# Kernel tuning notes

Measured on AMD Instinct MI355X. Metric: run time of the kernel, lower is better.

Reference implementation:

```python
import jax, jax.numpy as jnp
import numpy as np

HEADS = 8
DIM_HEAD = 64
INNER = HEADS * DIM_HEAD  # 512
EPS = 1e-6


def layer_norm(x, gamma, beta):
    mu = jnp.mean(x, axis=-1, keepdims=True)
    var = jnp.var(x, axis=-1, keepdims=True)
    return (x - mu) * jax.lax.rsqrt(var + EPS) * gamma + beta


def setup_inputs() -> dict:
    key = jax.random.key(0)
    ks = jax.random.split(key, 8)
    b, n = 2, 2048
    s = lambda d: 1.0 / np.sqrt(d)
    return {
        "x": jax.random.normal(ks[0], (b, n, INNER), dtype=jnp.float32),
        # weights stored input-major: y = x @ W
        "w_qkv": jax.random.normal(ks[1], (INNER, 3 * INNER), dtype=jnp.float32) * s(INNER),
        "w_out": jax.random.normal(ks[2], (INNER, INNER), dtype=jnp.float32) * s(INNER),
        "b_out": jax.random.normal(ks[3], (INNER,), dtype=jnp.float32) * 0.01,
        "w_ff1": jax.random.normal(ks[4], (INNER, 4 * INNER), dtype=jnp.float32) * s(INNER),
        "w_ff2": jax.random.normal(ks[5], (4 * INNER, INNER), dtype=jnp.float32) * s(4 * INNER),
        "g1": jnp.ones((INNER,), dtype=jnp.float32),
        "be1": jnp.zeros((INNER,), dtype=jnp.float32),
        "g2": jnp.ones((INNER,), dtype=jnp.float32),
        "be2": jnp.zeros((INNER,), dtype=jnp.float32),
    }


def reference(x, w_qkv, w_out, b_out, w_ff1, w_ff2, g1, be1, g2, be2):
    b, n, _ = x.shape
    scale = DIM_HEAD ** (-0.5)
    qkv = x @ w_qkv  # [b, n, 3*inner]
    qkv = qkv.reshape(b, n, 3, HEADS, DIM_HEAD)
    q = qkv[:, :, 0].transpose(0, 2, 1, 3)  # [b, h, n, d]
    k = qkv[:, :, 1].transpose(0, 2, 1, 3)
    v = qkv[:, :, 2].transpose(0, 2, 1, 3)
    dots = jnp.einsum('bhqd,bhkd->bhqk', q, k) * scale
    attn = jax.nn.softmax(dots, axis=-1)
    out = jnp.einsum('bhqk,bhkd->bhqd', attn, v)
    out = out.transpose(0, 2, 1, 3).reshape(b, n, INNER)
    out = out @ w_out + b_out
    attn_res = layer_norm(x + out, g1, be1)
    # NOTE: no activation between the two FFN linears (faithful to source)
    ff = (attn_res @ w_ff1) @ w_ff2
    return layer_norm(attn_res + ff, g2, be2)
```

## Files before the change

### kernel.cpp

```cpp
#include <hip/hip_runtime.h>
#include <hip/hip_bf16.h>
#include <cstdint>
#include <cstddef>
#include <math.h>

#define HEADS 8
#define DHEAD 64
#define INNER 512
#define BATCH 2
#define SEQ   2048
#define MROWS (BATCH*SEQ)
#define LN_EPS 1e-6f
#define KSPLIT 2
#define KCHUNK (SEQ/KSPLIT)

typedef unsigned short u16;
typedef __attribute__((ext_vector_type(8))) short short8;
typedef __attribute__((ext_vector_type(4))) float f32x4;

#define MFMA16(a,b,c) __builtin_amdgcn_mfma_f32_16x16x32_bf16((a),(b),(c),0,0,0)

__device__ __forceinline__ float bf2f(u16 u) {
    union { float f; uint32_t i; } x; x.i = ((uint32_t)u) << 16; return x.f;
}
__device__ __forceinline__ u16 f2bf(float f) {
    __hip_bfloat16 h = __float2bfloat16(f);
    return *reinterpret_cast<u16*>(&h);
}
__device__ __forceinline__ void gl_lds16(const void* g, void* l) {
    __builtin_amdgcn_global_load_lds(
        (const __attribute__((address_space(1))) void*)g,
        (__attribute__((address_space(3))) void*)l, 16, 0, 0);
}

__global__ void f32_to_bf16_kernel(const float* __restrict__ in,
                                   u16* __restrict__ out, int n4) {
    int i = (blockIdx.x * 256 + threadIdx.x);
    if (i < n4) {
        float4 v = reinterpret_cast<const float4*>(in)[i];
        ushort4 o;
        o.x = f2bf(v.x); o.y = f2bf(v.y); o.z = f2bf(v.z); o.w = f2bf(v.w);
        reinterpret_cast<ushort4*>(out)[i] = o;
    }
}

__global__ void transpose_to_bf16_kernel(const float* __restrict__ B,
                                         u16* __restrict__ Bt, int K, int N) {
    __shared__ float T[32][33];
    const int tid = threadIdx.x;
    const int n0 = blockIdx.x * 32, k0 = blockIdx.y * 32;
    const int r = tid >> 3, c = (tid & 7) * 4;
    float4 v = *reinterpret_cast<const float4*>(&B[(size_t)(k0 + r) * N + n0 + c]);
    T[c + 0][r] = v.x; T[c + 1][r] = v.y; T[c + 2][r] = v.z; T[c + 3][r] = v.w;
    __syncthreads();
    ushort4 o;
    o.x = f2bf(T[r][c + 0]); o.y = f2bf(T[r][c + 1]);
    o.z = f2bf(T[r][c + 2]); o.w = f2bf(T[r][c + 3]);
    *reinterpret_cast<ushort4*>(&Bt[(size_t)(n0 + r) * K + k0 + c]) = o;
}

template<int BN, int EPI>
__global__ __launch_bounds__(256) void gemm_bt(const u16* __restrict__ A,
                                               const u16* __restrict__ Bt,
                                               const float* __restrict__ bias,
                                               float* __restrict__ C,
                                               u16* __restrict__ Cb,
                                               u16* __restrict__ Vt,
                                               int M, int N, int K) {
    constexpr int WN = BN / 2;
    constexpr int NT = WN / 16;
    __shared__ u16 As[128 * 32];
    __shared__ u16 Bs[BN * 32];
    const int tid = threadIdx.x;
    const int wave = tid >> 6, lane = tid & 63;
    const int l15 = lane & 15, quad = lane >> 4;
    const int wm = (wave >> 1) * 64, wn = (wave & 1) * WN;
    const int row0 = blockIdx.y * 128, col0 = blockIdx.x * BN;

    int kbase = 0, kend = K;
    if (EPI == 3) {
        int chunk = K / gridDim.z;
        kbase = blockIdx.z * chunk; kend = kbase + chunk;
    }

    f32x4 acc[4][NT];
    #pragma unroll
    for (int mi = 0; mi < 4; ++mi)
        #pragma unroll
        for (int ni = 0; ni < NT; ++ni)
            #pragma unroll
            for (int e = 0; e < 4; ++e) acc[mi][ni][e] = 0.f;

    for (int k0 = kbase; k0 < kend; k0 += 32) {
        #pragma unroll
        for (int idx0 = 0; idx0 < 512 + BN * 4; idx0 += 256) {
            int idx = idx0 + tid;
            if (idx < 512) {
                int r = idx >> 2, ic = (idx & 3) * 8;
                gl_lds16(A + (size_t)(row0 + r) * K + k0 + ic, &As[idx * 8]);
            } else {
                int ib = idx - 512;
                int r = ib >> 2, ic = (ib & 3) * 8;
                gl_lds16(Bt + (size_t)(col0 + r) * K + k0 + ic, &Bs[ib * 8]);
            }
        }
        __syncthreads();

        short8 af[4], bf[NT];
        #pragma unroll
        for (int mi = 0; mi < 4; ++mi)
            af[mi] = *reinterpret_cast<const short8*>(&As[(wm + mi * 16 + l15) * 32 + quad * 8]);
        #pragma unroll
        for (int ni = 0; ni < NT; ++ni)
            bf[ni] = *reinterpret_cast<const short8*>(&Bs[(wn + ni * 16 + l15) * 32 + quad * 8]);
        #pragma unroll
        for (int mi = 0; mi < 4; ++mi)
            #pragma unroll
            for (int ni = 0; ni < NT; ++ni)
                acc[mi][ni] = MFMA16(af[mi], bf[ni], acc[mi][ni]);
        __syncthreads();
    }

    #pragma unroll
    for (int mi = 0; mi < 4; ++mi)
        #pragma unroll
        for (int ni = 0; ni < NT; ++ni) {
            const int cc = col0 + wn + ni * 16 + l15;
            const int rr0 = row0 + wm + mi * 16 + quad * 4;
            if (EPI == 0) {
                #pragma unroll
                for (int r = 0; r < 4; ++r)
                    Cb[(size_t)(rr0 + r) * N + cc] = f2bf(acc[mi][ni][r]);
            } else if (EPI == 1) {
                #pragma unroll
                for (int r = 0; r < 4; ++r)
                    C[(size_t)(rr0 + r) * N + cc] = acc[mi][ni][r] + bias[cc];
            } else if (EPI == 3) {
                float* Cz = C + (size_t)blockIdx.z * M * N;
                #pragma unroll
                for (int r = 0; r < 4; ++r)
                    Cz[(size_t)(rr0 + r) * N + cc] = acc[mi][ni][r];
            } else {
                if (cc < 1024) {
                    size_t base = (cc < 512) ? (size_t)cc
                                             : ((size_t)MROWS * 512 + cc - 512);
                    #pragma unroll
                    for (int r = 0; r < 4; ++r)
                        Cb[base + (size_t)(rr0 + r) * 512] = f2bf(acc[mi][ni][r]);
                } else {
                    int hh = (cc - 1024) >> 6, dd = (cc - 1024) & 63;
                    int bb = rr0 >> 11, srow = rr0 & 2047;
                    ushort4 o;
                    o.x = f2bf(acc[mi][ni][0]); o.y = f2bf(acc[mi][ni][1]);
                    o.z = f2bf(acc[mi][ni][2]); o.w = f2bf(acc[mi][ni][3]);
                    *reinterpret_cast<ushort4*>(
                        &Vt[(((size_t)(bb * 8 + hh) * 64 + dd) << 11) + srow]) = o;
                }
            }
        }
}

__global__ __launch_bounds__(256) void attn_kernel(const u16* __restrict__ qk_b,
                                                   const u16* __restrict__ vT_b,
                                                   float* __restrict__ Opart,
                                                   float* __restrict__ lpart) {
    __shared__ u16 QP[64][72];
    __shared__ u16 Ks[64][72];
    __shared__ u16 VT[64][72];

    const int tid = threadIdx.x;
    const int wave = tid >> 6, lane = tid & 63;
    const int l15 = lane & 15, quad = lane >> 4;
    const int qt = blockIdx.x, bh = blockIdx.y, ks = blockIdx.z;
    const int b = bh >> 3, h = bh & 7;
    const int w16 = wave * 16;
    const int r0 = tid >> 3, r1 = r0 + 32;
    const int ch = (tid & 7) * 8;

    {
        const u16* qb = qk_b + (size_t)(b * SEQ + qt * 64) * 512 + h * 64;
        *reinterpret_cast<uint4*>(&QP[r0][ch]) =
            *reinterpret_cast<const uint4*>(&qb[(size_t)r0 * 512 + ch]);
        *reinterpret_cast<uint4*>(&QP[r1][ch]) =
            *reinterpret_cast<const uint4*>(&qb[(size_t)r1 * 512 + ch]);
    }
    __syncthreads();

    short8 qf[2];
    qf[0] = *reinterpret_cast<const short8*>(&QP[w16 + l15][quad * 8]);
    qf[1] = *reinterpret_cast<const short8*>(&QP[w16 + l15][32 + quad * 8]);

    f32x4 oacc[4];
    float lsum[4];
    #pragma unroll
    for (int di = 0; di < 4; ++di)
        #pragma unroll
        for (int e = 0; e < 4; ++e) oacc[di][e] = 0.f;
    #pragma unroll
    for (int r = 0; r < 4; ++r) lsum[r] = 0.f;

    const u16* kb = qk_b + (size_t)MROWS * 512
                  + (size_t)(b * SEQ + ks * KCHUNK) * 512 + h * 64;
    const u16* vb = vT_b + (size_t)bh * 64 * 2048 + ks * KCHUNK;

    uint4 kr0 = *reinterpret_cast<const uint4*>(&kb[(size_t)r0 * 512 + ch]);
    uint4 kr1 = *reinterpret_cast<const uint4*>(&kb[(size_t)r1 * 512 + ch]);
    uint4 vr0 = *reinterpret_cast<const uint4*>(&vb[(size_t)r0 * 2048 + ch]);
    uint4 vr1 = *reinterpret_cast<const uint4*>(&vb[(size_t)r1 * 2048 + ch]);

    const float CEXP = 0.18033688011110918f;

    for (int kt = 0; kt < KCHUNK / 64; ++kt) {
        *reinterpret_cast<uint4*>(&Ks[r0][ch]) = kr0;
        *reinterpret_cast<uint4*>(&Ks[r1][ch]) = kr1;
        *reinterpret_cast<uint4*>(&VT[r0][ch]) = vr0;
        *reinterpret_cast<uint4*>(&VT[r1][ch]) = vr1;
        __syncthreads();

        if (kt + 1 < KCHUNK / 64) {
            const u16* kb2 = kb + (size_t)(kt + 1) * 64 * 512;
            const u16* vb2 = vb + (kt + 1) * 64;
            kr0 = *reinterpret_cast<const uint4*>(&kb2[(size_t)r0 * 512 + ch]);
            kr1 = *reinterpret_cast<const uint4*>(&kb2[(size_t)r1 * 512 + ch]);
            vr0 = *reinterpret_cast<const uint4*>(&vb2[(size_t)r0 * 2048 + ch]);
            vr1 = *reinterpret_cast<const uint4*>(&vb2[(size_t)r1 * 2048 + ch]);
        }

        f32x4 sacc[4];
        #pragma unroll
        for (int ni = 0; ni < 4; ++ni)
            #pragma unroll
            for (int e = 0; e < 4; ++e) sacc[ni][e] = 0.f;
        #pragma unroll
        for (int ksk = 0; ksk < 2; ++ksk) {
            short8 kf[4];
            #pragma unroll
            for (int ni = 0; ni < 4; ++ni)
                kf[ni] = *reinterpret_cast<const short8*>(
                    &Ks[ni * 16 + l15][ksk * 32 + quad * 8]);
            #pragma unroll
            for (int ni = 0; ni < 4; ++ni)
                sacc[ni] = MFMA16(qf[ksk], kf[ni], sacc[ni]);
        }

        #pragma unroll
        for (int ni = 0; ni < 4; ++ni)
            #pragma unroll
            for (int r = 0; r < 4; ++r) {
                float p = exp2f(sacc[ni][r] * CEXP);
                lsum[r] += p;
                QP[w16 + quad * 4 + r][ni * 16 + l15] = f2bf(p);
            }

        #pragma unroll
        for (int ksk = 0; ksk < 2; ++ksk) {
            short8 pf = *reinterpret_cast<const short8*>(
                &QP[w16 + l15][ksk * 32 + quad * 8]);
            #pragma unroll
            for (int di = 0; di < 4; ++di) {
                short8 vf = *reinterpret_cast<const short8*>(
                    &VT[di * 16 + l15][ksk * 32 + quad * 8]);
                oacc[di] = MFMA16(pf, vf, oacc[di]);
            }
        }
        __syncthreads();
    }

    #pragma unroll
    for (int r = 0; r < 4; ++r) {
        float v = lsum[r];
        v += __shfl_xor(v, 1); v += __shfl_xor(v, 2);
        v += __shfl_xor(v, 4); v += __shfl_xor(v, 8);
        lsum[r] = v;
    }

    const size_t pbase = ((size_t)(ks * 16 + bh) * SEQ + qt * 64);
    #pragma unroll
    for (int di = 0; di < 4; ++di)
        #pragma unroll
        for (int r = 0; r < 4; ++r)
            Opart[(pbase + w16 + quad * 4 + r) * 64 + di * 16 + l15] = oacc[di][r];
    if (l15 == 0)
        #pragma unroll
        for (int r = 0; r < 4; ++r)
            lpart[pbase + w16 + quad * 4 + r] = lsum[r];
}

__global__ void attn_combine_kernel(const float* __restrict__ Opart,
                                    const float* __restrict__ lpart,
                                    u16* __restrict__ attn_b) {
    int i = blockIdx.x * 256 + threadIdx.x;
    int e = i * 4;
    int row = e >> 9;
    int c = e & 511;
    int h = c >> 6, d = c & 63;
    int b = row >> 11, srow = row & 2047;
    int bh = b * 8 + h;

    size_t i0 = ((size_t)bh * SEQ + srow) * 64 + d;
    size_t i1 = ((size_t)(16 + bh) * SEQ + srow) * 64 + d;
    float4 o0 = *reinterpret_cast<const float4*>(&Opart[i0]);
    float4 o1 = *reinterpret_cast<const float4*>(&Opart[i1]);
    float l = lpart[(size_t)bh * SEQ + srow] + lpart[(size_t)(16 + bh) * SEQ + srow];
    float li = 1.f / l;
    ushort4 o;
    o.x = f2bf((o0.x + o1.x) * li);
    o.y = f2bf((o0.y + o1.y) * li);
    o.z = f2bf((o0.z + o1.z) * li);
    o.w = f2bf((o0.w + o1.w) * li);
    *reinterpret_cast<ushort4*>(&attn_b[(size_t)row * INNER + c]) = o;
}

template<bool A16, bool TWO>
__global__ void ln_kernel(const void* __restrict__ a_,
                          const float* __restrict__ s0,
                          const float* __restrict__ s1,
                          const float* __restrict__ g,
                          const float* __restrict__ be,
                          float* __restrict__ out32,
                          u16* __restrict__ out16) {
    __shared__ float red[256];
    const int row = blockIdx.x, tid = threadIdx.x;
    const size_t off = (size_t)row * INNER;
    const int c0 = tid, c1 = tid + 256;

    float a0, a1;
    if (A16) {
        const u16* a = (const u16*)a_;
        a0 = bf2f(a[off + c0]); a1 = bf2f(a[off + c1]);
    } else {
        const float* a = (const float*)a_;
        a0 = a[off + c0]; a1 = a[off + c1];
    }
    float v0 = a0 + s0[off + c0];
    float v1 = a1 + s0[off + c1];
    if (TWO) { v0 += s1[off + c0]; v1 += s1[off + c1]; }

    red[tid] = v0 + v1;
    __syncthreads();
    for (int s = 128; s > 0; s >>= 1) {
        if (tid < s) red[tid] += red[tid + s];
        __syncthreads();
    }
    float mu = red[0] * (1.f / INNER);
    __syncthreads();

    float d0 = v0 - mu, d1 = v1 - mu;
    red[tid] = d0 * d0 + d1 * d1;
    __syncthreads();
    for (int s = 128; s > 0; s >>= 1) {
        if (tid < s) red[tid] += red[tid + s];
        __syncthreads();
    }
    float rstd = rsqrtf(red[0] * (1.f / INNER) + LN_EPS);

    float y0 = d0 * rstd * g[c0] + be[c0];
    float y1 = d1 * rstd * g[c1] + be[c1];
    if (out32) { out32[off + c0] = y0; out32[off + c1] = y1; }
    if (out16) { out16[off + c0] = f2bf(y0); out16[off + c1] = f2bf(y1); }
}

extern "C" void kernel_launch(void* const* d_in, const int* in_sizes, int n_in,
                              void* d_out, int out_size, void* d_ws, size_t ws_size,
                              hipStream_t stream) {
    const float* x     = (const float*)d_in[0];
    const float* w_qkv = (const float*)d_in[1];
    const float* w_out = (const float*)d_in[2];
    const float* b_out = (const float*)d_in[3];
    const float* w_ff1 = (const float*)d_in[4];
    const float* w_ff2 = (const float*)d_in[5];
    const float* g1    = (const float*)d_in[6];
    const float* be1   = (const float*)d_in[7];
    const float* g2    = (const float*)d_in[8];
    const float* be2   = (const float*)d_in[9];
    float* out = (float*)d_out;

    char* W = (char*)d_ws;
    u16*   w_outT     = (u16*)  (W + 0);
    u16*   w_ff1T     = (u16*)  (W + 524288);
    u16*   w_ff2T     = (u16*)  (W + 2621440);
    u16*   qk_b       = (u16*)  (W + 4718592);
    u16*   attn_b     = (u16*)  (W + 4718592);
    u16*   attn_res_b = (u16*)  (W + 4718592);
    float* proj       = (float*)(W + 8912896);
    u16*   ff1_b      = (u16*)  (W + 8912896);
    u16*   vT_b       = (u16*)  (W + 13107200);
    u16*   x_b        = (u16*)  (W + 17301504);
    u16*   w_qkvT     = (u16*)  (W + 21495808);
    float* Opart      = (float*)(W + 17301504);
    float* lpart      = (float*)(W + 34078720);
    float* ff2p       = (float*)(W + 25690112);

    f32_to_bf16_kernel<<<(MROWS * INNER / 4 + 255) / 256, 256, 0, stream>>>(
        x, x_b, MROWS * INNER / 4);
    transpose_to_bf16_kernel<<<dim3(1536 / 32, 512 / 32),  256, 0, stream>>>(w_qkv, w_qkvT, 512, 1536);
    transpose_to_bf16_kernel<<<dim3(512 / 32,  512 / 32),  256, 0, stream>>>(w_out, w_outT, 512, 512);
    transpose_to_bf16_kernel<<<dim3(2048 / 32, 512 / 32),  256, 0, stream>>>(w_ff1, w_ff1T, 512, 2048);
    transpose_to_bf16_kernel<<<dim3(512 / 32,  2048 / 32), 256, 0, stream>>>(w_ff2, w_ff2T, 2048, 512);

    gemm_bt<128, 2><<<dim3(1536 / 128, MROWS / 128), 256, 0, stream>>>(
        x_b, w_qkvT, nullptr, nullptr, qk_b, vT_b, MROWS, 1536, INNER);

    attn_kernel<<<dim3(SEQ / 64, BATCH * HEADS, KSPLIT), 256, 0, stream>>>(
        qk_b, vT_b, Opart, lpart);

    attn_combine_kernel<<<(MROWS * INNER / 4) / 256, 256, 0, stream>>>(
        Opart, lpart, attn_b);

    gemm_bt<64, 1><<<dim3(INNER / 64, MROWS / 128), 256, 0, stream>>>(
        attn_b, w_outT, b_out, proj, nullptr, nullptr, MROWS, INNER, INNER);

    ln_kernel<false, false><<<MROWS, 256, 0, stream>>>(
        x, proj, nullptr, g1, be1, nullptr, attn_res_b);

    gemm_bt<128, 0><<<dim3(2048 / 128, MROWS / 128), 256, 0, stream>>>(
        attn_res_b, w_ff1T, nullptr, nullptr, ff1_b, nullptr, MROWS, 2048, INNER);

    gemm_bt<64, 3><<<dim3(INNER / 64, MROWS / 128, 2), 256, 0, stream>>>(
        ff1_b, w_ff2T, nullptr, ff2p, nullptr, nullptr, MROWS, INNER, 2048);

    ln_kernel<true, true><<<MROWS, 256, 0, stream>>>(
        attn_res_b, ff2p, ff2p + (size_t)MROWS * INNER, g2, be2, out, nullptr);
}
```

Measured before the change: 236.0 us.

## Fuse prep kernels, split attention keys four ways, keep P in registers

After: 223.6 us. 5.3% less time.

```diff
diff --git a/kernel.cpp b/kernel.cpp
--- a/kernel.cpp
+++ b/kernel.cpp
@@ -11,14 +11,19 @@
 #define SEQ   2048
 #define MROWS (BATCH*SEQ)
 #define LN_EPS 1e-6f
-#define KSPLIT 2
+#define KSPLIT 4
 #define KCHUNK (SEQ/KSPLIT)
 
 typedef unsigned short u16;
 typedef __attribute__((ext_vector_type(8))) short short8;
+typedef __attribute__((ext_vector_type(4))) short short4v;
 typedef __attribute__((ext_vector_type(4))) float f32x4;
 
 #define MFMA16(a,b,c) __builtin_amdgcn_mfma_f32_16x16x32_bf16((a),(b),(c),0,0,0)
+#if __has_builtin(__builtin_amdgcn_mfma_f32_16x16x16bf16_1k)
+#define HAVE_MFMA16K16 1
+#define MFMA16K16(a,b,c) __builtin_amdgcn_mfma_f32_16x16x16bf16_1k((a),(b),(c),0,0,0)
+#endif
 
 __device__ __forceinline__ float bf2f(u16 u) {
     union { float f; uint32_t i; } x; x.i = ((uint32_t)u) << 16; return x.f;
@@ -33,22 +38,28 @@
         (__attribute__((address_space(3))) void*)l, 16, 0, 0);
 }
 
-__global__ void f32_to_bf16_kernel(const float* __restrict__ in,
-                                   u16* __restrict__ out, int n4) {
-    int i = (blockIdx.x * 256 + threadIdx.x);
-    if (i < n4) {
-        float4 v = reinterpret_cast<const float4*>(in)[i];
+__global__ void prep_kernel(const float* __restrict__ x, u16* __restrict__ x_b,
+                            const float* __restrict__ w_qkv, u16* __restrict__ w_qkvT,
+                            const float* __restrict__ w_out, u16* __restrict__ w_outT,
+                            const float* __restrict__ w_ff1, u16* __restrict__ w_ff1T,
+                            const float* __restrict__ w_ff2, u16* __restrict__ w_ff2T) {
+    __shared__ float T[32][33];
+    const int blk = blockIdx.x, tid = threadIdx.x;
+    if (blk < 2048) {
+        int i = blk * 256 + tid;
+        float4 v = reinterpret_cast<const float4*>(x)[i];
         ushort4 o;
         o.x = f2bf(v.x); o.y = f2bf(v.y); o.z = f2bf(v.z); o.w = f2bf(v.w);
-        reinterpret_cast<ushort4*>(out)[i] = o;
-    }
-}
-
-__global__ void transpose_to_bf16_kernel(const float* __restrict__ B,
-                                         u16* __restrict__ Bt, int K, int N) {
-    __shared__ float T[32][33];
-    const int tid = threadIdx.x;
-    const int n0 = blockIdx.x * 32, k0 = blockIdx.y * 32;
+        reinterpret_cast<ushort4*>(x_b)[i] = o;
+        return;
+    }
+    const float* B; u16* Bt; int K, N, t;
+    if (blk < 2816)      { B = w_qkv; Bt = w_qkvT; K = 512;  N = 1536; t = blk - 2048; }
+    else if (blk < 3072) { B = w_out; Bt = w_outT; K = 512;  N = 512;  t = blk - 2816; }
+    else if (blk < 4096) { B = w_ff1; Bt = w_ff1T; K = 512;  N = 2048; t = blk - 3072; }
+    else                 { B = w_ff2; Bt = w_ff2T; K = 2048; N = 512;  t = blk - 4096; }
+    const int nb = N / 32;
+    const int n0 = (t % nb) * 32, k0 = (t / nb) * 32;
     const int r = tid >> 3, c = (tid & 7) * 4;
     float4 v = *reinterpret_cast<const float4*>(&B[(size_t)(k0 + r) * N + n0 + c]);
     T[c + 0][r] = v.x; T[c + 1][r] = v.y; T[c + 2][r] = v.z; T[c + 3][r] = v.w;
@@ -162,11 +173,12 @@
 
 __global__ __launch_bounds__(256) void attn_kernel(const u16* __restrict__ qk_b,
                                                    const u16* __restrict__ vT_b,
-                                                   float* __restrict__ Opart,
+                                                   u16* __restrict__ OpartB,
                                                    float* __restrict__ lpart) {
-    __shared__ u16 QP[64][72];
-    __shared__ u16 Ks[64][72];
-    __shared__ u16 VT[64][72];
+    __shared__ u16 SM[3 * 64 * 72];
+    u16 (*Qs)[72] = (u16(*)[72])SM;
+    u16 (*Ks)[72] = (u16(*)[72])(SM + 64 * 72);
+    u16 (*VT)[72] = (u16(*)[72])(SM + 2 * 64 * 72);
 
     const int tid = threadIdx.x;
     const int wave = tid >> 6, lane = tid & 63;
@@ -179,25 +191,16 @@
 
     {
         const u16* qb = qk_b + (size_t)(b * SEQ + qt * 64) * 512 + h * 64;
-        *reinterpret_cast<uint4*>(&QP[r0][ch]) =
+        *reinterpret_cast<uint4*>(&Qs[r0][ch]) =
             *reinterpret_cast<const uint4*>(&qb[(size_t)r0 * 512 + ch]);
-        *reinterpret_cast<uint4*>(&QP[r1][ch]) =
+        *reinterpret_cast<uint4*>(&Qs[r1][ch]) =
             *reinterpret_cast<const uint4*>(&qb[(size_t)r1 * 512 + ch]);
     }
     __syncthreads();
 
     short8 qf[2];
-    qf[0] = *reinterpret_cast<const short8*>(&QP[w16 + l15][quad * 8]);
-    qf[1] = *reinterpret_cast<const short8*>(&QP[w16 + l15][32 + quad * 8]);
-
-    f32x4 oacc[4];
-    float lsum[4];
-    #pragma unroll
-    for (int di = 0; di < 4; ++di)
-        #pragma unroll
-        for (int e = 0; e < 4; ++e) oacc[di][e] = 0.f;
-    #pragma unroll
-    for (int r = 0; r < 4; ++r) lsum[r] = 0.f;
+    qf[0] = *reinterpret_cast<const short8*>(&Qs[w16 + l15][quad * 8]);
+    qf[1] = *reinterpret_cast<const short8*>(&Qs[w16 + l15][32 + quad * 8]);
 
     const u16* kb = qk_b + (size_t)MROWS * 512
                   + (size_t)(b * SEQ + ks * KCHUNK) * 512 + h * 64;
@@ -209,6 +212,14 @@
     uint4 vr1 = *reinterpret_cast<const uint4*>(&vb[(size_t)r1 * 2048 + ch]);
 
     const float CEXP = 0.18033688011110918f;
+
+#ifdef HAVE_MFMA16K16
+    f32x4 oacc[4];
+    float lsum = 0.f;
+    #pragma unroll
+    for (int di = 0; di < 4; ++di)
+        #pragma unroll
+        for (int e = 0; e < 4; ++e) oacc[di][e] = 0.f;
 
     for (int kt = 0; kt < KCHUNK / 64; ++kt) {
         *reinterpret_cast<uint4*>(&Ks[r0][ch]) = kr0;
@@ -240,22 +251,103 @@
                     &Ks[ni * 16 + l15][ksk * 32 + quad * 8]);
             #pragma unroll
             for (int ni = 0; ni < 4; ++ni)
+                sacc[ni] = MFMA16(kf[ni], qf[ksk], sacc[ni]);
+        }
+
+        #pragma unroll
+        for (int ni = 0; ni < 4; ++ni) {
+            short4v pp;
+            #pragma unroll
+            for (int r = 0; r < 4; ++r) {
+                float p = exp2f(sacc[ni][r] * CEXP);
+                lsum += p;
+                pp[r] = (short)f2bf(p);
+            }
+            #pragma unroll
+            for (int di = 0; di < 4; ++di) {
+                short4v vf = *reinterpret_cast<const short4v*>(
+                    &VT[di * 16 + l15][ni * 16 + quad * 4]);
+                oacc[di] = MFMA16K16(vf, pp, oacc[di]);
+            }
+        }
+        __syncthreads();
+    }
+
+    lsum += __shfl_xor(lsum, 16);
+    lsum += __shfl_xor(lsum, 32);
+
+    const size_t pbase = ((size_t)(ks * 16 + bh) * SEQ + qt * 64);
+    if (lane < 16) lpart[pbase + w16 + lane] = lsum;
+
+    float* OTf = (float*)SM;
+    #pragma unroll
+    for (int di = 0; di < 4; ++di)
+        #pragma unroll
+        for (int r = 0; r < 4; ++r)
+            OTf[(di * 16 + quad * 4 + r) * 68 + w16 + l15] = oacc[di][r];
+    __syncthreads();
+
+    const int ql = tid >> 2, dseg = (tid & 3) * 16;
+    u16 ov[16];
+    #pragma unroll
+    for (int i = 0; i < 16; ++i) ov[i] = f2bf(OTf[(dseg + i) * 68 + ql]);
+    u16* op = &OpartB[(pbase + ql) * 64 + dseg];
+    *reinterpret_cast<uint4*>(op)     = *reinterpret_cast<const uint4*>(ov);
+    *reinterpret_cast<uint4*>(op + 8) = *reinterpret_cast<const uint4*>(ov + 8);
+#else
+    f32x4 oacc[4];
+    float lsum[4];
+    #pragma unroll
+    for (int di = 0; di < 4; ++di)
+        #pragma unroll
+        for (int e = 0; e < 4; ++e) oacc[di][e] = 0.f;
+    #pragma unroll
+    for (int r = 0; r < 4; ++r) lsum[r] = 0.f;
+
+    for (int kt = 0; kt < KCHUNK / 64; ++kt) {
+        *reinterpret_cast<uint4*>(&Ks[r0][ch]) = kr0;
+        *reinterpret_cast<uint4*>(&Ks[r1][ch]) = kr1;
+        *reinterpret_cast<uint4*>(&VT[r0][ch]) = vr0;
+        *reinterpret_cast<uint4*>(&VT[r1][ch]) = vr1;
+        __syncthreads();
+
+        if (kt + 1 < KCHUNK / 64) {
+            const u16* kb2 = kb + (size_t)(kt + 1) * 64 * 512;
+            const u16* vb2 = vb + (kt + 1) * 64;
+            kr0 = *reinterpret_cast<const uint4*>(&kb2[(size_t)r0 * 512 + ch]);
+            kr1 = *reinterpret_cast<const uint4*>(&kb2[(size_t)r1 * 512 + ch]);
+            vr0 = *reinterpret_cast<const uint4*>(&vb2[(size_t)r0 * 2048 + ch]);
+            vr1 = *reinterpret_cast<const uint4*>(&vb2[(size_t)r1 * 2048 + ch]);
+        }
+
+        f32x4 sacc[4];
+        #pragma unroll
+        for (int ni = 0; ni < 4; ++ni)
+            #pragma unroll
+            for (int e = 0; e < 4; ++e) sacc[ni][e] = 0.f;
+        #pragma unroll
+        for (int ksk = 0; ksk < 2; ++ksk) {
+            short8 kf[4];
+            #pragma unroll
+            for (int ni = 0; ni < 4; ++ni)
+                kf[ni] = *reinterpret_cast<const short8*>(
+                    &Ks[ni * 16 + l15][ksk * 32 + quad * 8]);
+            #pragma unroll
+            for (int ni = 0; ni < 4; ++ni)
                 sacc[ni] = MFMA16(qf[ksk], kf[ni], sacc[ni]);
         }
-
         #pragma unroll
         for (int ni = 0; ni < 4; ++ni)
             #pragma unroll
             for (int r = 0; r < 4; ++r) {
                 float p = exp2f(sacc[ni][r] * CEXP);
                 lsum[r] += p;
-                QP[w16 + quad * 4 + r][ni * 16 + l15] = f2bf(p);
+                Qs[w16 + quad * 4 + r][ni * 16 + l15] = f2bf(p);
             }
-
         #pragma unroll
         for (int ksk = 0; ksk < 2; ++ksk) {
             short8 pf = *reinterpret_cast<const short8*>(
-                &QP[w16 + l15][ksk * 32 + quad * 8]);
+                &Qs[w16 + l15][ksk * 32 + quad * 8]);
             #pragma unroll
             for (int di = 0; di < 4; ++di) {
                 short8 vf = *reinterpret_cast<const short8*>(
@@ -273,20 +365,20 @@
         v += __shfl_xor(v, 4); v += __shfl_xor(v, 8);
         lsum[r] = v;
     }
-
     const size_t pbase = ((size_t)(ks * 16 + bh) * SEQ + qt * 64);
     #pragma unroll
     for (int di = 0; di < 4; ++di)
         #pragma unroll
         for (int r = 0; r < 4; ++r)
-            Opart[(pbase + w16 + quad * 4 + r) * 64 + di * 16 + l15] = oacc[di][r];
+            OpartB[(pbase + w16 + quad * 4 + r) * 64 + di * 16 + l15] = f2bf(oacc[di][r]);
     if (l15 == 0)
         #pragma unroll
         for (int r = 0; r < 4; ++r)
             lpart[pbase + w16 + quad * 4 + r] = lsum[r];
-}
-
-__global__ void attn_combine_kernel(const float* __restrict__ Opart,
+#endif
+}
+
+__global__ void attn_combine_kernel(const u16* __restrict__ OpartB,
                                     const float* __restrict__ lpart,
                                     u16* __restrict__ attn_b) {
     int i = blockIdx.x * 256 + threadIdx.x;
@@ -297,17 +389,18 @@
     int b = row >> 11, srow = row & 2047;
     int bh = b * 8 + h;
 
-    size_t i0 = ((size_t)bh * SEQ + srow) * 64 + d;
-    size_t i1 = ((size_t)(16 + bh) * SEQ + srow) * 64 + d;
-    float4 o0 = *reinterpret_cast<const float4*>(&Opart[i0]);
-    float4 o1 = *reinterpret_cast<const float4*>(&Opart[i1]);
-    float l = lpart[(size_t)bh * SEQ + srow] + lpart[(size_t)(16 + bh) * SEQ + srow];
+    float ax = 0.f, ay = 0.f, az = 0.f, aw = 0.f, l = 0.f;
+    #pragma unroll
+    for (int ks = 0; ks < KSPLIT; ++ks) {
+        size_t pk = (size_t)(ks * 16 + bh) * SEQ + srow;
+        ushort4 o = *reinterpret_cast<const ushort4*>(&OpartB[pk * 64 + d]);
+        ax += bf2f(o.x); ay += bf2f(o.y); az += bf2f(o.z); aw += bf2f(o.w);
+        l += lpart[pk];
+    }
     float li = 1.f / l;
     ushort4 o;
-    o.x = f2bf((o0.x + o1.x) * li);
-    o.y = f2bf((o0.y + o1.y) * li);
-    o.z = f2bf((o0.z + o1.z) * li);
-    o.w = f2bf((o0.w + o1.w) * li);
+    o.x = f2bf(ax * li); o.y = f2bf(ay * li);
+    o.z = f2bf(az * li); o.w = f2bf(aw * li);
     *reinterpret_cast<ushort4*>(&attn_b[(size_t)row * INNER + c]) = o;
 }
 
@@ -387,25 +480,21 @@
     u16*   vT_b       = (u16*)  (W + 13107200);
     u16*   x_b        = (u16*)  (W + 17301504);
     u16*   w_qkvT     = (u16*)  (W + 21495808);
-    float* Opart      = (float*)(W + 17301504);
+    u16*   OpartB     = (u16*)  (W + 17301504);
     float* lpart      = (float*)(W + 34078720);
     float* ff2p       = (float*)(W + 25690112);
 
-    f32_to_bf16_kernel<<<(MROWS * INNER / 4 + 255) / 256, 256, 0, stream>>>(
-        x, x_b, MROWS * INNER / 4);
-    transpose_to_bf16_kernel<<<dim3(1536 / 32, 512 / 32),  256, 0, stream>>>(w_qkv, w_qkvT, 512, 1536);
-    transpose_to_bf16_kernel<<<dim3(512 / 32,  512 / 32),  256, 0, stream>>>(w_out, w_outT, 512, 512);
-    transpose_to_bf16_kernel<<<dim3(2048 / 32, 512 / 32),  256, 0, stream>>>(w_ff1, w_ff1T, 512, 2048);
-    transpose_to_bf16_kernel<<<dim3(512 / 32,  2048 / 32), 256, 0, stream>>>(w_ff2, w_ff2T, 2048, 512);
+    prep_kernel<<<5120, 256, 0, stream>>>(x, x_b, w_qkv, w_qkvT, w_out, w_outT,
+                                          w_ff1, w_ff1T, w_ff2, w_ff2T);
 
     gemm_bt<128, 2><<<dim3(1536 / 128, MROWS / 128), 256, 0, stream>>>(
         x_b, w_qkvT, nullptr, nullptr, qk_b, vT_b, MROWS, 1536, INNER);
 
     attn_kernel<<<dim3(SEQ / 64, BATCH * HEADS, KSPLIT), 256, 0, stream>>>(
-        qk_b, vT_b, Opart, lpart);
+        qk_b, vT_b, OpartB, lpart);
 
     attn_combine_kernel<<<(MROWS * INNER / 4) / 256, 256, 0, stream>>>(
-        Opart, lpart, attn_b);
+        OpartB, lpart, attn_b);
 
     gemm_bt<64, 1><<<dim3(INNER / 64, MROWS / 128), 256, 0, stream>>>(
         attn_b, w_outT, b_out, proj, nullptr, nullptr, MROWS, INNER, INNER);
```
